# Performance work log

Measured on AMD Instinct MI355X. Metric: run time of the kernel, lower is better.

The kernel has to match this reference:

```python
import jax, jax.numpy as jnp
import numpy as np

TRUNK = 128  # hard-coded trunk_size in the Triton kernels


def setup_inputs() -> dict:
    key = jax.random.key(0)
    kq, kk, kv = jax.random.split(key, 3)
    N, D = 262144, 64
    Q = jax.random.normal(kq, (N, D), dtype=jnp.float32)
    K = jax.random.normal(kk, (N, D), dtype=jnp.float32)
    V = jax.random.normal(kv, (N, D), dtype=jnp.float32)
    return {"Q": Q, "K": K, "V": V}


def reference(Q, K, V):
    # Faithful to the Triton module:
    # 1) intra kernel overwrites Q in-place with, per trunk t:
    #      Q_t <- Q_t @ (V_t^T K_t)^T = Q_t @ K_t^T @ V_t
    # 2) inter kernel accumulates global state S = sum_t V_t^T K_t = V^T K (fp32)
    # 3) final output = Q_intra @ S
    N, D = Q.shape
    dtype = Q.dtype
    assert N % TRUNK == 0
    T = N // TRUNK
    Qt = Q.reshape(T, TRUNK, D)
    Kt = K.reshape(T, TRUNK, D)
    Vt = V.reshape(T, TRUNK, D)
    # per-trunk scores [T, TRUNK, TRUNK], then apply to V
    scores = jnp.einsum('tnd,tmd->tnm', Qt, Kt)
    Q_intra = jnp.einsum('tnm,tmd->tnd', scores, Vt).reshape(N, D)
    # global DxD state in float32 (atomic_add accumulator dtype)
    S = jnp.einsum('nd,ne->de', V.astype(jnp.float32), K.astype(jnp.float32))
    out = Q_intra @ S.astype(dtype)
    return out
```

## Files before the change

### kernel.cpp

```cpp
#include <hip/hip_runtime.h>
#include <hip/hip_bf16.h>


#define TRUNK 128
#define DD 64

typedef __bf16 bf16x8 __attribute__((ext_vector_type(8)));
typedef float  f32x4  __attribute__((ext_vector_type(4)));
typedef unsigned int   u32;
typedef unsigned short u16;
typedef u32 u32x4 __attribute__((ext_vector_type(4)));
typedef u32 u32x2 __attribute__((ext_vector_type(2)));

union F8 { bf16x8 v; u16 u[8]; u32x4 q; };

__device__ __forceinline__ u16 f2bf(float x) {
    union { float f; u32 u; } a; a.f = x;
    u32 u = a.u;
    return (u16)((u + 0x7FFFu + ((u >> 16) & 1u)) >> 16);
}
__device__ __forceinline__ u32 pack2(float a, float b) {
    return (u32)f2bf(a) | ((u32)f2bf(b) << 16);
}

#define P_S  72
#define KV_T 136

__device__ __forceinline__ void stage_T256(const float* __restrict__ M, long tb,
                                           u16* __restrict__ MT, int t) {
    const int c0 = (t >> 4) * 4;
    const int r0 = (t & 15) * 8;
    float4 rw[8];
    #pragma unroll
    for (int i = 0; i < 8; ++i)
        rw[i] = *(const float4*)(M + tb + (long)(r0 + i) * 64 + c0);
    #pragma unroll
    for (int j = 0; j < 4; ++j) {
        u32x4 w;
        w[0] = pack2(((const float*)&rw[0])[j], ((const float*)&rw[1])[j]);
        w[1] = pack2(((const float*)&rw[2])[j], ((const float*)&rw[3])[j]);
        w[2] = pack2(((const float*)&rw[4])[j], ((const float*)&rw[5])[j]);
        w[3] = pack2(((const float*)&rw[6])[j], ((const float*)&rw[7])[j]);
        *(u32x4*)&MT[(c0 + j) * KV_T + r0] = w;
    }
}

__global__ __launch_bounds__(256, 4) void g_kernel(const float* __restrict__ K,
                                                   const float* __restrict__ V,
                                                   u16* __restrict__ G,
                                                   float* __restrict__ S) {
    __shared__ __align__(16) u16 lds[2 * 64 * KV_T];
    u16* KT = lds;
    u16* VT = lds + 64 * KV_T;

    const int t    = threadIdx.x;
    const int lane = t & 63;
    const int wave = t >> 6;
    const int l15  = lane & 15;
    const int quad = lane >> 4;
    const int mt0  = (wave >> 1) << 1;
    const int nt0  = (wave & 1) << 1;

    const int  tt = blockIdx.x;
    const long tb = (long)tt * (TRUNK * DD);

    stage_T256(K, tb, KT, t);
    stage_T256(V, tb, VT, t);
    __syncthreads();

    f32x4 gacc[2][2] = {};
    #pragma unroll
    for (int kt = 0; kt < 4; ++kt) {
        const int rbase = kt * 32 + quad * 8;
        F8 af[2], bf[2];
        #pragma unroll
        for (int mi = 0; mi < 2; ++mi)
            af[mi].q = *(const u32x4*)&VT[((mt0 + mi) * 16 + l15) * KV_T + rbase];
        #pragma unroll
        for (int ni = 0; ni < 2; ++ni)
            bf[ni].q = *(const u32x4*)&KT[((nt0 + ni) * 16 + l15) * KV_T + rbase];
        #pragma unroll
        for (int mi = 0; mi < 2; ++mi)
            #pragma unroll
            for (int ni = 0; ni < 2; ++ni)
                gacc[mi][ni] = __builtin_amdgcn_mfma_f32_16x16x32_bf16(
                    af[mi].v, bf[ni].v, gacc[mi][ni], 0, 0, 0);
    }

    u16* Gt = G + ((size_t)(tt >> 1) * 32768 + (size_t)(tt & 1) * 4096);
    #pragma unroll
    for (int mi = 0; mi < 2; ++mi)
        #pragma unroll
        for (int ni = 0; ni < 2; ++ni) {
            const int ga  = (nt0 + ni) * 16 + l15;
            const int gb0 = (mt0 + mi) * 16 + quad * 4;
            const float* g = (const float*)&gacc[mi][ni];
            u32x2 w; w[0] = pack2(g[0], g[1]); w[1] = pack2(g[2], g[3]);
            *(u32x2*)&Gt[ga * 64 + gb0] = w;
        }

    #pragma unroll
    for (int mi = 0; mi < 2; ++mi)
        #pragma unroll
        for (int ni = 0; ni < 2; ++ni) {
            const int b0 = (mt0 + mi) * 16 + quad * 4;
            const int a  = (nt0 + ni) * 16 + l15;
            const float* g = (const float*)&gacc[mi][ni];
            #pragma unroll
            for (int reg = 0; reg < 4; ++reg)
                atomicAdd(&S[(b0 + reg) * 64 + a], g[reg]);
        }
}

#define LDS3 (2 * 64 * P_S)

__global__ __launch_bounds__(256, 3) void out_kernel(const float* __restrict__ Q,
                                                     const float* __restrict__ S,
                                                     const u16* __restrict__ G,
                                                     float* __restrict__ out) {
    __shared__ __align__(16) u16 lds[LDS3];
    u16* STb = lds;
    u16* HTb = lds + 64 * P_S;

    const int t    = threadIdx.x;
    const int lane = t & 63;
    const int wave = t >> 6;
    const int l15  = lane & 15;
    const int quad = lane >> 4;
    const int mt0  = (wave >> 1) << 1;
    const int nt0  = (wave & 1) << 1;

    const u16* Gblk = G + (size_t)blockIdx.x * 32768;
    F8 gf[2][2][2];
    #pragma unroll
    for (int tr = 0; tr < 2; ++tr)
        #pragma unroll
        for (int kt = 0; kt < 2; ++kt)
            #pragma unroll
            for (int mi = 0; mi < 2; ++mi)
                gf[tr][kt][mi].q = *(const u32x4*)&Gblk[(size_t)tr * 4096 +
                    ((mt0 + mi) * 16 + l15) * 64 + kt * 32 + quad * 8];

    {
        const int sb0 = (t & 7) * 8;
        const int sc0 = (t >> 3) * 2;
        float2 sv[8];
        #pragma unroll
        for (int i = 0; i < 8; ++i)
            sv[i] = *(const float2*)(S + (sb0 + i) * 64 + sc0);
        #pragma unroll
        for (int j = 0; j < 2; ++j) {
            u32x4 w;
            w[0] = pack2(((const float*)&sv[0])[j], ((const float*)&sv[1])[j]);
            w[1] = pack2(((const float*)&sv[2])[j], ((const float*)&sv[3])[j]);
            w[2] = pack2(((const float*)&sv[4])[j], ((const float*)&sv[5])[j]);
            w[3] = pack2(((const float*)&sv[6])[j], ((const float*)&sv[7])[j]);
            *(u32x4*)&STb[(sc0 + j) * P_S + sb0] = w;
        }
    }
    asm volatile("s_waitcnt vmcnt(0)" ::: "memory");
    __syncthreads();

    #pragma unroll
    for (int tr = 0; tr < 2; ++tr) {
        const long tb = ((long)blockIdx.x * 2 + tr) * (TRUNK * DD);

        F8 a3[2][2];
        #pragma unroll
        for (int kt = 0; kt < 2; ++kt)
            #pragma unroll
            for (int mi = 0; mi < 2; ++mi) {
                const int r = (wave * 2 + mi) * 16 + l15;
                const float* qp = Q + tb + r * 64 + kt * 32 + quad * 8;
                float4 q0 = *(const float4*)qp;
                float4 q1 = *(const float4*)(qp + 4);
                a3[kt][mi].q[0] = pack2(q0.x, q0.y);
                a3[kt][mi].q[1] = pack2(q0.z, q0.w);
                a3[kt][mi].q[2] = pack2(q1.x, q1.y);
                a3[kt][mi].q[3] = pack2(q1.z, q1.w);
            }

        f32x4 hacc[2][2] = {};
        #pragma unroll
        for (int kt = 0; kt < 2; ++kt) {
            const int kb = kt * 32 + quad * 8;
            F8 b2[2];
            #pragma unroll
            for (int ni = 0; ni < 2; ++ni)
                b2[ni].q = *(const u32x4*)&STb[((nt0 + ni) * 16 + l15) * P_S + kb];
            #pragma unroll
            for (int mi = 0; mi < 2; ++mi)
                #pragma unroll
                for (int ni = 0; ni < 2; ++ni)
                    hacc[mi][ni] = __builtin_amdgcn_mfma_f32_16x16x32_bf16(
                        gf[tr][kt][mi].v, b2[ni].v, hacc[mi][ni], 0, 0, 0);
        }
        #pragma unroll
        for (int mi = 0; mi < 2; ++mi)
            #pragma unroll
            for (int ni = 0; ni < 2; ++ni) {
                const int hc  = (nt0 + ni) * 16 + l15;
                const int ha0 = (mt0 + mi) * 16 + quad * 4;
                const float* h = (const float*)&hacc[mi][ni];
                u32x2 w; w[0] = pack2(h[0], h[1]); w[1] = pack2(h[2], h[3]);
                *(u32x2*)&HTb[hc * P_S + ha0] = w;
            }
        __syncthreads();

        f32x4 oacc[2][4] = {};
        #pragma unroll
        for (int kt = 0; kt < 2; ++kt) {
            const int ka = kt * 32 + quad * 8;
            #pragma unroll
            for (int ni = 0; ni < 4; ++ni) {
                F8 bb;
                bb.q = *(const u32x4*)&HTb[(ni * 16 + l15) * P_S + ka];
                #pragma unroll
                for (int mi = 0; mi < 2; ++mi)
                    oacc[mi][ni] = __builtin_amdgcn_mfma_f32_16x16x32_bf16(
                        a3[kt][mi].v, bb.v, oacc[mi][ni], 0, 0, 0);
            }
        }
        #pragma unroll
        for (int mi = 0; mi < 2; ++mi)
            #pragma unroll
            for (int ni = 0; ni < 4; ++ni) {
                const int row0 = (wave * 2 + mi) * 16 + quad * 4;
                const int col  = ni * 16 + l15;
                const float* o = (const float*)&oacc[mi][ni];
                #pragma unroll
                for (int reg = 0; reg < 4; ++reg)
                    out[tb + (long)(row0 + reg) * 64 + col] = o[reg];
            }
        if (tr == 0) __syncthreads();
    }
}

extern "C" void kernel_launch(void* const* d_in, const int* in_sizes, int n_in,
                              void* d_out, int out_size, void* d_ws, size_t ws_size,
                              hipStream_t stream) {
    const float* Q = (const float*)d_in[0];
    const float* K = (const float*)d_in[1];
    const float* V = (const float*)d_in[2];
    float* out = (float*)d_out;
    float* S   = (float*)d_ws;

    const int n = in_sizes[0] / DD;
    const int T = n / TRUNK;

    u16* G = (u16*)out;

    hipMemsetAsync(S, 0, DD * DD * sizeof(float), stream);
    g_kernel<<<T, 256, 0, stream>>>(K, V, G, S);
    out_kernel<<<T / 2, 256, 0, stream>>>(Q, S, G, out);
}
```

Measured before the change: 238.9 us.

## Replace per-trunk S atomics with block partials plus separate reduction kernel

g_kernel now processes two trunks per block, loads K/V straight from global memory into MFMA fragments instead of staging transposed tiles in LDS, and sums the two trunk Gram matrices in registers. Instead of atomically adding every block's partial into S, each block writes its partial S into unused space in the output buffer, and a new s_reduce kernel sums the partials with far fewer atomics. This aims to cut heavy atomic contention on the 64x64 S, at the cost of an extra kernel launch, strided uncoalesced global loads, and extra partial-buffer traffic.

```diff
diff --git a/kernel.cpp b/kernel.cpp
--- a/kernel.cpp
+++ b/kernel.cpp
@@ -24,35 +24,10 @@
 }
 
 #define P_S  72
-#define KV_T 136
-
-__device__ __forceinline__ void stage_T256(const float* __restrict__ M, long tb,
-                                           u16* __restrict__ MT, int t) {
-    const int c0 = (t >> 4) * 4;
-    const int r0 = (t & 15) * 8;
-    float4 rw[8];
-    #pragma unroll
-    for (int i = 0; i < 8; ++i)
-        rw[i] = *(const float4*)(M + tb + (long)(r0 + i) * 64 + c0);
-    #pragma unroll
-    for (int j = 0; j < 4; ++j) {
-        u32x4 w;
-        w[0] = pack2(((const float*)&rw[0])[j], ((const float*)&rw[1])[j]);
-        w[1] = pack2(((const float*)&rw[2])[j], ((const float*)&rw[3])[j]);
-        w[2] = pack2(((const float*)&rw[4])[j], ((const float*)&rw[5])[j]);
-        w[3] = pack2(((const float*)&rw[6])[j], ((const float*)&rw[7])[j]);
-        *(u32x4*)&MT[(c0 + j) * KV_T + r0] = w;
-    }
-}
 
 __global__ __launch_bounds__(256, 4) void g_kernel(const float* __restrict__ K,
                                                    const float* __restrict__ V,
-                                                   u16* __restrict__ G,
-                                                   float* __restrict__ S) {
-    __shared__ __align__(16) u16 lds[2 * 64 * KV_T];
-    u16* KT = lds;
-    u16* VT = lds + 64 * KV_T;
-
+                                                   float* __restrict__ outb) {
     const int t    = threadIdx.x;
     const int lane = t & 63;
     const int wave = t >> 6;
@@ -61,55 +36,91 @@
     const int mt0  = (wave >> 1) << 1;
     const int nt0  = (wave & 1) << 1;
 
-    const int  tt = blockIdx.x;
-    const long tb = (long)tt * (TRUNK * DD);
-
-    stage_T256(K, tb, KT, t);
-    stage_T256(V, tb, VT, t);
-    __syncthreads();
-
-    f32x4 gacc[2][2] = {};
-    #pragma unroll
-    for (int kt = 0; kt < 4; ++kt) {
-        const int rbase = kt * 32 + quad * 8;
-        F8 af[2], bf[2];
+    const int am0 = (mt0 + 0) * 16 + l15;
+    const int am1 = (mt0 + 1) * 16 + l15;
+    const int bn0 = (nt0 + 0) * 16 + l15;
+    const int bn1 = (nt0 + 1) * 16 + l15;
+
+    u16* G = (u16*)outb;
+    f32x4 sacc[2][2] = {};
+
+    #pragma unroll
+    for (int tr = 0; tr < 2; ++tr) {
+        const int  tt = blockIdx.x * 2 + tr;
+        const long tb = (long)tt * (TRUNK * DD);
+        const float* Vb = V + tb + (long)quad * 8 * 64;
+        const float* Kb = K + tb + (long)quad * 8 * 64;
+
+        f32x4 gacc[2][2] = {};
+        #pragma unroll
+        for (int kt = 0; kt < 4; ++kt) {
+            const int ro = kt * 32 * 64;
+            float a0[8], a1[8], b0[8], b1[8];
+            #pragma unroll
+            for (int i = 0; i < 8; ++i) {
+                a0[i] = Vb[ro + i * 64 + am0];
+                a1[i] = Vb[ro + i * 64 + am1];
+                b0[i] = Kb[ro + i * 64 + bn0];
+                b1[i] = Kb[ro + i * 64 + bn1];
+            }
+            F8 af[2], bf[2];
+            #pragma unroll
+            for (int j = 0; j < 4; ++j) {
+                af[0].q[j] = pack2(a0[2 * j], a0[2 * j + 1]);
+                af[1].q[j] = pack2(a1[2 * j], a1[2 * j + 1]);
+                bf[0].q[j] = pack2(b0[2 * j], b0[2 * j + 1]);
+                bf[1].q[j] = pack2(b1[2 * j], b1[2 * j + 1]);
+            }
+            gacc[0][0] = __builtin_amdgcn_mfma_f32_16x16x32_bf16(af[0].v, bf[0].v, gacc[0][0], 0, 0, 0);
+            gacc[0][1] = __builtin_amdgcn_mfma_f32_16x16x32_bf16(af[0].v, bf[1].v, gacc[0][1], 0, 0, 0);
+            gacc[1][0] = __builtin_amdgcn_mfma_f32_16x16x32_bf16(af[1].v, bf[0].v, gacc[1][0], 0, 0, 0);
+            gacc[1][1] = __builtin_amdgcn_mfma_f32_16x16x32_bf16(af[1].v, bf[1].v, gacc[1][1], 0, 0, 0);
+        }
+
+        u16* Gt = G + ((size_t)(tt >> 1) * 32768 + (size_t)(tt & 1) * 4096);
         #pragma unroll
         for (int mi = 0; mi < 2; ++mi)
-            af[mi].q = *(const u32x4*)&VT[((mt0 + mi) * 16 + l15) * KV_T + rbase];
-        #pragma unroll
-        for (int ni = 0; ni < 2; ++ni)
-            bf[ni].q = *(const u32x4*)&KT[((nt0 + ni) * 16 + l15) * KV_T + rbase];
-        #pragma unroll
-        for (int mi = 0; mi < 2; ++mi)
-            #pragma unroll
-            for (int ni = 0; ni < 2; ++ni)
-                gacc[mi][ni] = __builtin_amdgcn_mfma_f32_16x16x32_bf16(
-                    af[mi].v, bf[ni].v, gacc[mi][ni], 0, 0, 0);
-    }
-
-    u16* Gt = G + ((size_t)(tt >> 1) * 32768 + (size_t)(tt & 1) * 4096);
-    #pragma unroll
-    for (int mi = 0; mi < 2; ++mi)
-        #pragma unroll
-        for (int ni = 0; ni < 2; ++ni) {
-            const int ga  = (nt0 + ni) * 16 + l15;
-            const int gb0 = (mt0 + mi) * 16 + quad * 4;
-            const float* g = (const float*)&gacc[mi][ni];
-            u32x2 w; w[0] = pack2(g[0], g[1]); w[1] = pack2(g[2], g[3]);
-            *(u32x2*)&Gt[ga * 64 + gb0] = w;
-        }
-
+            #pragma unroll
+            for (int ni = 0; ni < 2; ++ni) {
+                const int ga  = (nt0 + ni) * 16 + l15;
+                const int gb0 = (mt0 + mi) * 16 + quad * 4;
+                const float* g = (const float*)&gacc[mi][ni];
+                u32x2 w; w[0] = pack2(g[0], g[1]); w[1] = pack2(g[2], g[3]);
+                *(u32x2*)&Gt[ga * 64 + gb0] = w;
+                sacc[mi][ni] += gacc[mi][ni];
+            }
+    }
+
+    float* o = outb + (size_t)blockIdx.x * 16384 + 4096;
     #pragma unroll
     for (int mi = 0; mi < 2; ++mi)
         #pragma unroll
         for (int ni = 0; ni < 2; ++ni) {
             const int b0 = (mt0 + mi) * 16 + quad * 4;
             const int a  = (nt0 + ni) * 16 + l15;
-            const float* g = (const float*)&gacc[mi][ni];
+            const float* g = (const float*)&sacc[mi][ni];
             #pragma unroll
             for (int reg = 0; reg < 4; ++reg)
-                atomicAdd(&S[(b0 + reg) * 64 + a], g[reg]);
-        }
+                o[(b0 + reg) * 64 + a] = g[reg];
+        }
+}
+
+__global__ __launch_bounds__(256) void s_reduce(const float* __restrict__ Pb,
+                                                float* __restrict__ S) {
+    const int tid = blockIdx.x * 256 + threadIdx.x;
+    const int eg  = tid & 1023;
+    const int way = tid >> 10;
+    const float4* p = (const float4*)Pb;
+    float4 acc = {0.f, 0.f, 0.f, 0.f};
+    #pragma unroll 4
+    for (int i = 0; i < 16; ++i) {
+        float4 v = p[(size_t)(way * 16 + i) * 4096 + 1024 + eg];
+        acc.x += v.x; acc.y += v.y; acc.z += v.z; acc.w += v.w;
+    }
+    atomicAdd(&S[eg * 4 + 0], acc.x);
+    atomicAdd(&S[eg * 4 + 1], acc.y);
+    atomicAdd(&S[eg * 4 + 2], acc.z);
+    atomicAdd(&S[eg * 4 + 3], acc.w);
 }
 
 #define LDS3 (2 * 64 * P_S)
@@ -251,6 +262,7 @@
     u16* G = (u16*)out;
 
     hipMemsetAsync(S, 0, DD * DD * sizeof(float), stream);
-    g_kernel<<<T, 256, 0, stream>>>(K, V, G, S);
+    g_kernel<<<T / 2, 256, 0, stream>>>(K, V, out);
+    s_reduce<<<256, 256, 0, stream>>>(out, S);
     out_kernel<<<T / 2, 256, 0, stream>>>(Q, S, G, out);
 }
```

After: 256.4 us. 7.3% more time.

## Process four trunks per block with register prefetch and hierarchical S reduction

Applied to the files above, without the earlier changes.

The G kernel now handles four trunks per block. It prefetches the next trunk's K/V into registers while computing the current one, and accumulates the partial V^T K state in registers. Instead of global atomics from every block, each block writes its partial 64x64 sum into unused space in the output buffer, and a new small reduce kernel sums these with far fewer atomics. This removes heavy atomic contention on S but adds a kernel launch, fewer blocks and lower occupancy.

```diff
diff --git a/kernel.cpp b/kernel.cpp
--- a/kernel.cpp
+++ b/kernel.cpp
@@ -26,14 +26,18 @@
 #define P_S  72
 #define KV_T 136
 
-__device__ __forceinline__ void stage_T256(const float* __restrict__ M, long tb,
-                                           u16* __restrict__ MT, int t) {
+__device__ __forceinline__ void load_T(const float* __restrict__ M, long tb,
+                                       int t, float4 rw[8]) {
     const int c0 = (t >> 4) * 4;
     const int r0 = (t & 15) * 8;
-    float4 rw[8];
     #pragma unroll
     for (int i = 0; i < 8; ++i)
         rw[i] = *(const float4*)(M + tb + (long)(r0 + i) * 64 + c0);
+}
+__device__ __forceinline__ void write_T(u16* __restrict__ MT, int t,
+                                        const float4 rw[8]) {
+    const int c0 = (t >> 4) * 4;
+    const int r0 = (t & 15) * 8;
     #pragma unroll
     for (int j = 0; j < 4; ++j) {
         u32x4 w;
@@ -45,10 +49,9 @@
     }
 }
 
-__global__ __launch_bounds__(256, 4) void g_kernel(const float* __restrict__ K,
-                                                   const float* __restrict__ V,
-                                                   u16* __restrict__ G,
-                                                   float* __restrict__ S) {
+__global__ __launch_bounds__(256, 2) void gs_kernel(const float* __restrict__ K,
+                                                    const float* __restrict__ V,
+                                                    float* __restrict__ outb) {
     __shared__ __align__(16) u16 lds[2 * 64 * KV_T];
     u16* KT = lds;
     u16* VT = lds + 64 * KV_T;
@@ -61,55 +64,97 @@
     const int mt0  = (wave >> 1) << 1;
     const int nt0  = (wave & 1) << 1;
 
-    const int  tt = blockIdx.x;
-    const long tb = (long)tt * (TRUNK * DD);
-
-    stage_T256(K, tb, KT, t);
-    stage_T256(V, tb, VT, t);
-    __syncthreads();
-
-    f32x4 gacc[2][2] = {};
-    #pragma unroll
-    for (int kt = 0; kt < 4; ++kt) {
-        const int rbase = kt * 32 + quad * 8;
-        F8 af[2], bf[2];
+    u16* G = (u16*)outb;
+    f32x4 sacc[2][2] = {};
+
+    const long base = (long)blockIdx.x * 4 * (TRUNK * DD);
+
+    float4 kreg[8], vreg[8];
+    load_T(K, base, t, kreg);
+    load_T(V, base, t, vreg);
+    write_T(KT, t, kreg);
+    write_T(VT, t, vreg);
+
+    #pragma unroll
+    for (int c = 0; c < 4; ++c) {
+        __syncthreads();
+
+        if (c < 3) {
+            const long nb = base + (long)(c + 1) * (TRUNK * DD);
+            load_T(K, nb, t, kreg);
+            load_T(V, nb, t, vreg);
+        }
+
+        f32x4 gacc[2][2] = {};
+        #pragma unroll
+        for (int kt = 0; kt < 4; ++kt) {
+            const int rbase = kt * 32 + quad * 8;
+            F8 af[2], bf[2];
+            #pragma unroll
+            for (int mi = 0; mi < 2; ++mi)
+                af[mi].q = *(const u32x4*)&VT[((mt0 + mi) * 16 + l15) * KV_T + rbase];
+            #pragma unroll
+            for (int ni = 0; ni < 2; ++ni)
+                bf[ni].q = *(const u32x4*)&KT[((nt0 + ni) * 16 + l15) * KV_T + rbase];
+            #pragma unroll
+            for (int mi = 0; mi < 2; ++mi)
+                #pragma unroll
+                for (int ni = 0; ni < 2; ++ni)
+                    gacc[mi][ni] = __builtin_amdgcn_mfma_f32_16x16x32_bf16(
+                        af[mi].v, bf[ni].v, gacc[mi][ni], 0, 0, 0);
+        }
+
+        const int tt = blockIdx.x * 4 + c;
+        u16* Gt = G + ((size_t)(tt >> 1) * 32768 + (size_t)(tt & 1) * 4096);
         #pragma unroll
         for (int mi = 0; mi < 2; ++mi)
-            af[mi].q = *(const u32x4*)&VT[((mt0 + mi) * 16 + l15) * KV_T + rbase];
-        #pragma unroll
-        for (int ni = 0; ni < 2; ++ni)
-            bf[ni].q = *(const u32x4*)&KT[((nt0 + ni) * 16 + l15) * KV_T + rbase];
-        #pragma unroll
-        for (int mi = 0; mi < 2; ++mi)
-            #pragma unroll
-            for (int ni = 0; ni < 2; ++ni)
-                gacc[mi][ni] = __builtin_amdgcn_mfma_f32_16x16x32_bf16(
-                    af[mi].v, bf[ni].v, gacc[mi][ni], 0, 0, 0);
-    }
-
-    u16* Gt = G + ((size_t)(tt >> 1) * 32768 + (size_t)(tt & 1) * 4096);
-    #pragma unroll
-    for (int mi = 0; mi < 2; ++mi)
-        #pragma unroll
-        for (int ni = 0; ni < 2; ++ni) {
-            const int ga  = (nt0 + ni) * 16 + l15;
-            const int gb0 = (mt0 + mi) * 16 + quad * 4;
-            const float* g = (const float*)&gacc[mi][ni];
-            u32x2 w; w[0] = pack2(g[0], g[1]); w[1] = pack2(g[2], g[3]);
-            *(u32x2*)&Gt[ga * 64 + gb0] = w;
-        }
-
+            #pragma unroll
+            for (int ni = 0; ni < 2; ++ni) {
+                const int ga  = (nt0 + ni) * 16 + l15;
+                const int gb0 = (mt0 + mi) * 16 + quad * 4;
+                const float* g = (const float*)&gacc[mi][ni];
+                u32x2 w; w[0] = pack2(g[0], g[1]); w[1] = pack2(g[2], g[3]);
+                *(u32x2*)&Gt[ga * 64 + gb0] = w;
+                sacc[mi][ni] += gacc[mi][ni];
+            }
+
+        __syncthreads();
+        if (c < 3) {
+            write_T(KT, t, kreg);
+            write_T(VT, t, vreg);
+        }
+    }
+
+    float* o = outb + (size_t)blockIdx.x * 16384 + 4096;
     #pragma unroll
     for (int mi = 0; mi < 2; ++mi)
         #pragma unroll
         for (int ni = 0; ni < 2; ++ni) {
             const int b0 = (mt0 + mi) * 16 + quad * 4;
             const int a  = (nt0 + ni) * 16 + l15;
-            const float* g = (const float*)&gacc[mi][ni];
+            const float* g = (const float*)&sacc[mi][ni];
             #pragma unroll
             for (int reg = 0; reg < 4; ++reg)
-                atomicAdd(&S[(b0 + reg) * 64 + a], g[reg]);
-        }
+                o[(b0 + reg) * 64 + a] = g[reg];
+        }
+}
+
+__global__ __launch_bounds__(256) void s_reduce(const float* __restrict__ Pb,
+                                                float* __restrict__ S) {
+    const int tid = blockIdx.x * 256 + threadIdx.x;
+    const int eg  = tid & 1023;
+    const int way = tid >> 10;
+    const float4* p = (const float4*)Pb;
+    float4 acc = {0.f, 0.f, 0.f, 0.f};
+    #pragma unroll 4
+    for (int i = 0; i < 16; ++i) {
+        float4 v = p[(size_t)(way * 16 + i) * 4096 + 1024 + eg];
+        acc.x += v.x; acc.y += v.y; acc.z += v.z; acc.w += v.w;
+    }
+    atomicAdd(&S[eg * 4 + 0], acc.x);
+    atomicAdd(&S[eg * 4 + 1], acc.y);
+    atomicAdd(&S[eg * 4 + 2], acc.z);
+    atomicAdd(&S[eg * 4 + 3], acc.w);
 }
 
 #define LDS3 (2 * 64 * P_S)
@@ -251,6 +296,7 @@
     u16* G = (u16*)out;
 
     hipMemsetAsync(S, 0, DD * DD * sizeof(float), stream);
-    g_kernel<<<T, 256, 0, stream>>>(K, V, G, S);
+    gs_kernel<<<T / 4, 256, 0, stream>>>(K, V, out);
+    s_reduce<<<128, 256, 0, stream>>>(out, S);
     out_kernel<<<T / 2, 256, 0, stream>>>(Q, S, G, out);
 }
```

Result: no change. 236.0 us (-1.2%).
